# Kernel tuning notes

Hardware: AMD Instinct MI355X
Metric: run time of the kernel (lower is better)

The kernel has to match this reference:

```python
import jax, jax.numpy as jnp
import numpy as np

L = 0.24          # lambda step size
K = 0.03          # exp(log 0.03), conductance scale used by forward
NITER = 500       # ctor Niter
DEPS = 0.1


def _g(x, k):
    # Perona-Malik conductance: 1 / (1 + |x^2| / k^2); x real so |x*x| == x*x
    return 1.0 / (1.0 + (x * x) / (k * k))


def setup_inputs() -> dict:
    key = jax.random.key(0)
    k1, k2 = jax.random.split(key)
    guide = jax.random.normal(k1, (2, 3, 512, 512), dtype=jnp.float32)
    initial = jax.random.uniform(k2, (2, 1, 512, 512), dtype=jnp.float32)
    return {"guide": guide, "initial": initial}


def reference(guide, initial):
    # shift branch (jit-safe): forward adds deps if initial.min() <= deps, subtracts at end
    shift = jnp.where(jnp.min(initial) <= DEPS, DEPS, 0.0).astype(initial.dtype)
    depth0 = initial + shift

    # conductance coefficients from guide (mean abs channel gradient), shapes:
    # cv: [B,1,H-1,W], ch: [B,1,H,W-1]
    cv = _g(jnp.mean(jnp.abs(guide[:, :, 1:, :] - guide[:, :, :-1, :]), axis=1, keepdims=True), K)
    ch = _g(jnp.mean(jnp.abs(guide[:, :, :, 1:] - guide[:, :, :, :-1]), axis=1, keepdims=True), K)

    def step(I, _):
        # both diffs computed from the same I (matches torch: dv, dh read before writes;
        # the in-place +/- updates commute, so functional adds give identical math)
        dv = I[:, :, 1:, :] - I[:, :, :-1, :]
        dh = I[:, :, :, 1:] - I[:, :, :, :-1]
        tv = L * cv * dv
        th = L * ch * dh
        I = I.at[:, :, 1:, :].add(-tv)
        I = I.at[:, :, :-1, :].add(tv)
        I = I.at[:, :, :, 1:].add(-th)
        I = I.at[:, :, :, :-1].add(th)
        return I, None

    depth, _ = jax.lax.scan(step, depth0, None, length=NITER)
    y_pred = depth - shift
    return (y_pred, cv, ch)
```

## Files before the change

### kernel.cpp

```cpp
#include <hip/hip_runtime.h>


#define HH 512
#define WW 512
#define NB 2
static constexpr float LAM   = 0.24f;
static constexpr float KCOND = 0.03f;
static constexpr float DEPS_ = 0.1f;
static constexpr int IMG      = HH * WW;
static constexpr int N_DEPTH  = NB * IMG;
static constexpr int CV_PER_B = (HH - 1) * WW;
static constexpr int CH_PER_B = HH * (WW - 1);
static constexpr int N_CV     = NB * CV_PER_B;
static constexpr int N_CH     = NB * CH_PER_B;

static constexpr int T_FUSE = 10, NSS = 50;
static constexpr int TILE_W = 64, TILE_H = 32;
static constexpr int HALO_X = 12, HALO_Y = 10;
static constexpr int RW = TILE_W + 2 * HALO_X;
static constexpr int RH = TILE_H + 2 * HALO_Y;
static constexpr int NQ_ROW = RW / 4;
static constexpr int NQUAD  = NQ_ROW * RH;
static constexpr int SSZ    = (RH + 2) * RW;

static constexpr int NU_ROW = RW / 4;
static constexpr int NU_COL = RH / 2;
static constexpr int NUNIT  = NU_ROW * NU_COL;
static constexpr int NTF    = 576;

static constexpr int S_LDS    = 92;
static constexpr int ROWS_SZ  = (RH + 2) * S_LDS;
static constexpr int TRASH_OFF = ROWS_SZ;
static constexpr int EDGE_OFF = ROWS_SZ + S_LDS;
static constexpr int EDGE_ENT = 580;
static constexpr int BUF_SZ   = EDGE_OFF + EDGE_ENT * 4;

static constexpr int CVW = RW;
static constexpr int CV_SZ = (RH + 1) * CVW;
static constexpr int CHW = RW + 8;
static constexpr int CH_SZ = RH * CHW;
static constexpr int BLOB_BLK = CV_SZ + CH_SZ;

static constexpr int QPT_F = 5;

__device__ __forceinline__ unsigned fkey(float f) {
    unsigned u = __float_as_uint(f);
    return (u & 0x80000000u) ? ~u : (u | 0x80000000u);
}
__device__ __forceinline__ float kinv(unsigned k) {
    return __uint_as_float((k & 0x80000000u) ? (k & 0x7fffffffu) : ~k);
}

__global__ void init_key_kernel(unsigned* key) { *key = 0xFFFFFFFFu; }

__global__ void min_kernel(const float* __restrict__ x, unsigned* key) {
    float m = 3.4e38f;
    for (int idx = blockIdx.x * blockDim.x + threadIdx.x; idx < N_DEPTH;
         idx += gridDim.x * blockDim.x)
        m = fminf(m, x[idx]);
    for (int off = 32; off > 0; off >>= 1) m = fminf(m, __shfl_down(m, off, 64));
    __shared__ float sm[4];
    int lane = threadIdx.x & 63, wv = threadIdx.x >> 6;
    if (lane == 0) sm[wv] = m;
    __syncthreads();
    if (threadIdx.x == 0) {
        float mm = fminf(fminf(sm[0], sm[1]), fminf(sm[2], sm[3]));
        atomicMin(key, fkey(mm));
    }
}

__global__ void coeff_kernel(const float* __restrict__ g, float* __restrict__ cv,
                             float* __restrict__ chh) {
    int idx = blockIdx.x * blockDim.x + threadIdx.x;
    constexpr float kk = KCOND * KCOND;
    if (idx < N_CV) {
        int b = idx / CV_PER_B;
        int r = idx - b * CV_PER_B;
        int i = r >> 9, j = r & (WW - 1);
        const float* gb = g + b * 3 * IMG + i * WW + j;
        float s = 0.f;
#pragma unroll
        for (int c = 0; c < 3; ++c) s += fabsf(gb[c * IMG + WW] - gb[c * IMG]);
        float m = s / 3.0f;
        cv[idx] = 1.0f / (1.0f + (m * m) / kk);
    } else if (idx < N_CV + N_CH) {
        int t = idx - N_CV;
        int b = t / CH_PER_B;
        int r = t - b * CH_PER_B;
        int i = r / (WW - 1);
        int j = r - i * (WW - 1);
        const float* gb = g + b * 3 * IMG + i * WW + j;
        float s = 0.f;
#pragma unroll
        for (int c = 0; c < 3; ++c) s += fabsf(gb[c * IMG + 1] - gb[c * IMG]);
        float m = s / 3.0f;
        chh[t] = 1.0f / (1.0f + (m * m) / kk);
    }
}

__global__ __launch_bounds__(256) void prep_planes(const float* __restrict__ cv_g,
                                                   const float* __restrict__ ch_g,
                                                   float* __restrict__ blob) {
    const int blk = blockIdx.x;
    const int b   = blk >> 7, t = blk & 127;
    const int y0  = (t >> 3) * TILE_H;
    const int x0  = (t & 7) * TILE_W;
    const float* cvb = cv_g + b * CV_PER_B;
    const float* chb = ch_g + b * CH_PER_B;
    float* pv = blob + blk * BLOB_BLK;
    float* ph = pv + CV_SZ;
    for (int i = threadIdx.x; i < CV_SZ; i += 256) {
        int rr = i / CVW, x = i - rr * CVW;
        int gy = y0 - HALO_Y + rr, gx = x0 - HALO_X + x;
        bool ok = (rr >= 1) && (rr <= RH - 1) && (gy >= 1) && (gy <= HH - 1) &&
                  (gx >= 0) && (gx < WW);
        pv[i] = ok ? LAM * cvb[(gy - 1) * WW + gx] : 0.f;
    }
    for (int i = threadIdx.x; i < CH_SZ; i += 256) {
        int rr = i / CHW, xe = i - rr * CHW;
        int gy = y0 - HALO_Y + rr, gxe = x0 - HALO_X + xe;
        bool ok = (xe >= 1) && (xe <= RW - 1) && (gy >= 0) && (gy < HH) &&
                  (gxe >= 1) && (gxe < WW);
        ph[i] = ok ? LAM * chb[gy * (WW - 1) + (gxe - 1)] : 0.f;
    }
}

template <bool ADD_SHIFT, bool SUB_SHIFT>
__global__ __launch_bounds__(NTF, 1) void step_fast(
    const float* __restrict__ src, float* __restrict__ dst,
    const float* __restrict__ blob, const unsigned* __restrict__ key) {
    __shared__ float sb[2][BUF_SZ];
    const int blk = blockIdx.x;
    const int b   = blk >> 7, t = blk & 127;
    const int y0  = (t >> 3) * TILE_H;
    const int x0  = (t & 7) * TILE_W;
    const float* srcb = src + b * IMG;
    const float* pv   = blob + blk * BLOB_BLK;
    const float* ph   = pv + CV_SZ;

    float shift = 0.f;
    if (ADD_SHIFT || SUB_SHIFT) shift = (kinv(*key) <= DEPS_) ? DEPS_ : 0.f;
    const int tid = threadIdx.x;

    const bool act = tid < NUNIT;
    const int  uc  = act ? tid : 0;
    const int  pr  = uc / NU_ROW;
    const int  px  = uc - pr * NU_ROW;
    const int  x   = px * 4;
    const int  r0  = 2 * pr, r1 = r0 + 1;
    int roff0 = (r0 + 1) * S_LDS + x;
    int roff1 = roff0 + S_LDS;
    if (!act) {
        roff0 = TRASH_OFF + (tid & 3) * 8;
        roff1 = roff0 + 4;
    }
    const int e_w  = EDGE_OFF + (tid + 1) * 4;
    const int e_lf = EDGE_OFF + tid * 4 + 2;
    const int e_rt = EDGE_OFF + (tid + 2) * 4;

    const int gy0 = y0 - HALO_Y + r0, gy1 = gy0 + 1;
    const int gx  = x0 - HALO_X + x;
    const bool gx_in = (gx >= 0) && (gx <= WW - 4);
    const bool in0 = act && gx_in && (gy0 >= 0) && (gy0 < HH);
    const bool in1 = act && gx_in && (gy1 >= 0) && (gy1 < HH);
    const int goff0 = in0 ? (gy0 * WW + gx) : 0;
    const int goff1 = in1 ? (gy1 * WW + gx) : 0;
    const bool is_int = act && (r0 >= HALO_Y) && (r1 < HALO_Y + TILE_H) &&
                        (x >= HALO_X) && (x < HALO_X + TILE_W);

    const float am = act ? 1.f : 0.f;
    float ca[4], cm[4], cb[4], h0[5], h1[5];
    {
        float4 a = *reinterpret_cast<const float4*>(&pv[r0 * CVW + x]);
        float4 m = *reinterpret_cast<const float4*>(&pv[r1 * CVW + x]);
        float4 d = *reinterpret_cast<const float4*>(&pv[(r1 + 1) * CVW + x]);
        ca[0] = a.x * am; ca[1] = a.y * am; ca[2] = a.z * am; ca[3] = a.w * am;
        cm[0] = m.x * am; cm[1] = m.y * am; cm[2] = m.z * am; cm[3] = m.w * am;
        cb[0] = d.x * am; cb[1] = d.y * am; cb[2] = d.z * am; cb[3] = d.w * am;
        float4 u = *reinterpret_cast<const float4*>(&ph[r0 * CHW + x]);
        float  u4 = ph[r0 * CHW + x + 4];
        float4 w = *reinterpret_cast<const float4*>(&ph[r1 * CHW + x]);
        float  w4 = ph[r1 * CHW + x + 4];
        h0[0] = u.x * am; h0[1] = u.y * am; h0[2] = u.z * am; h0[3] = u.w * am; h0[4] = u4 * am;
        h1[0] = w.x * am; h1[1] = w.y * am; h1[2] = w.z * am; h1[3] = w.w * am; h1[4] = w4 * am;
    }

    float v0[4] = {0.f, 0.f, 0.f, 0.f}, v1[4] = {0.f, 0.f, 0.f, 0.f};
    if (in0) {
        float4 tv = *reinterpret_cast<const float4*>(srcb + goff0);
        if (ADD_SHIFT) { tv.x += shift; tv.y += shift; tv.z += shift; tv.w += shift; }
        v0[0] = tv.x; v0[1] = tv.y; v0[2] = tv.z; v0[3] = tv.w;
    }
    if (in1) {
        float4 tv = *reinterpret_cast<const float4*>(srcb + goff1);
        if (ADD_SHIFT) { tv.x += shift; tv.y += shift; tv.z += shift; tv.w += shift; }
        v1[0] = tv.x; v1[1] = tv.y; v1[2] = tv.z; v1[3] = tv.w;
    }

    for (int i = tid; i < S_LDS; i += NTF) {
        sb[0][i] = 0.f; sb[0][(RH + 1) * S_LDS + i] = 0.f;
        sb[1][i] = 0.f; sb[1][(RH + 1) * S_LDS + i] = 0.f;
    }
    if (tid == 0) {
        float4 z{0.f, 0.f, 0.f, 0.f};
        *reinterpret_cast<float4*>(&sb[0][EDGE_OFF]) = z;
        *reinterpret_cast<float4*>(&sb[1][EDGE_OFF]) = z;
        *reinterpret_cast<float4*>(&sb[0][EDGE_OFF + 577 * 4]) = z;
        *reinterpret_cast<float4*>(&sb[1][EDGE_OFF + 577 * 4]) = z;
    }
    *reinterpret_cast<float4*>(&sb[0][roff0]) = float4{v0[0], v0[1], v0[2], v0[3]};
    *reinterpret_cast<float4*>(&sb[0][roff1]) = float4{v1[0], v1[1], v1[2], v1[3]};
    *reinterpret_cast<float4*>(&sb[0][e_w])   = float4{v0[0], v1[0], v0[3], v1[3]};
    __syncthreads();

    int cur = 0;
    for (int it = 0; it < T_FUSE; ++it) {
        const float* s = sb[cur];
        float2 lfp = *reinterpret_cast<const float2*>(&s[e_lf]);
        float2 rtp = *reinterpret_cast<const float2*>(&s[e_rt]);
        float4 up = *reinterpret_cast<const float4*>(&s[roff0 - S_LDS]);
        float4 dn = *reinterpret_cast<const float4*>(&s[roff1 + S_LDS]);

        float n0[4], n1[4];
        n0[0] = v0[0] - ca[0] * (v0[0] - up.x) + cm[0] * (v1[0] - v0[0])
                      - h0[0] * (v0[0] - lfp.x) + h0[1] * (v0[1] - v0[0]);
        n0[1] = v0[1] - ca[1] * (v0[1] - up.y) + cm[1] * (v1[1] - v0[1])
                      - h0[1] * (v0[1] - v0[0]) + h0[2] * (v0[2] - v0[1]);
        n0[2] = v0[2] - ca[2] * (v0[2] - up.z) + cm[2] * (v1[2] - v0[2])
                      - h0[2] * (v0[2] - v0[1]) + h0[3] * (v0[3] - v0[2]);
        n0[3] = v0[3] - ca[3] * (v0[3] - up.w) + cm[3] * (v1[3] - v0[3])
                      - h0[3] * (v0[3] - v0[2]) + h0[4] * (rtp.x - v0[3]);
        n1[0] = v1[0] - cm[0] * (v1[0] - v0[0]) + cb[0] * (dn.x - v1[0])
                      - h1[0] * (v1[0] - lfp.y) + h1[1] * (v1[1] - v1[0]);
        n1[1] = v1[1] - cm[1] * (v1[1] - v0[1]) + cb[1] * (dn.y - v1[1])
                      - h1[1] * (v1[1] - v1[0]) + h1[2] * (v1[2] - v1[1]);
        n1[2] = v1[2] - cm[2] * (v1[2] - v0[2]) + cb[2] * (dn.z - v1[2])
                      - h1[2] * (v1[2] - v1[1]) + h1[3] * (v1[3] - v1[2]);
        n1[3] = v1[3] - cm[3] * (v1[3] - v0[3]) + cb[3] * (dn.w - v1[3])
                      - h1[3] * (v1[3] - v1[2]) + h1[4] * (rtp.y - v1[3]);

        int nxt = cur ^ 1;
        float* d = sb[nxt];
        *reinterpret_cast<float4*>(&d[roff0]) = float4{n0[0], n0[1], n0[2], n0[3]};
        *reinterpret_cast<float4*>(&d[roff1]) = float4{n1[0], n1[1], n1[2], n1[3]};
        *reinterpret_cast<float4*>(&d[e_w])   = float4{n0[0], n1[0], n0[3], n1[3]};
        v0[0] = n0[0]; v0[1] = n0[1]; v0[2] = n0[2]; v0[3] = n0[3];
        v1[0] = n1[0]; v1[1] = n1[1]; v1[2] = n1[2]; v1[3] = n1[3];
        cur = nxt;
        __syncthreads();
    }

    float* dstb = dst + b * IMG;
    if (is_int) {
        float4 o0{v0[0], v0[1], v0[2], v0[3]};
        float4 o1{v1[0], v1[1], v1[2], v1[3]};
        if (SUB_SHIFT) {
            o0.x -= shift; o0.y -= shift; o0.z -= shift; o0.w -= shift;
            o1.x -= shift; o1.y -= shift; o1.z -= shift; o1.w -= shift;
        }
        *reinterpret_cast<float4*>(dstb + goff0) = o0;
        *reinterpret_cast<float4*>(dstb + goff1) = o1;
    }
}

template <bool ADD_SHIFT, bool SUB_SHIFT>
__global__ __launch_bounds__(256, 1) void step_fused(
    const float* __restrict__ src, float* __restrict__ dst,
    const float* __restrict__ cv_g, const float* __restrict__ ch_g,
    const unsigned* __restrict__ key) {
    __shared__ float sb[2][SSZ];
    const int blk = blockIdx.x;
    const int b = blk >> 7, t = blk & 127;
    const int y0 = (t >> 3) * TILE_H, x0 = (t & 7) * TILE_W;
    const float* cvb = cv_g + b * CV_PER_B;
    const float* chb = ch_g + b * CH_PER_B;
    const float* srcb = src + b * IMG;
    float* dstb = dst + b * IMG;
    float shift = 0.f;
    if (ADD_SHIFT || SUB_SHIFT) shift = (kinv(*key) <= DEPS_) ? DEPS_ : 0.f;
    const int tid = threadIdx.x;
    float v[QPT_F][4], cu[QPT_F][4], cd[QPT_F][4], chq[QPT_F][5];
    int roff[QPT_F], rr[QPT_F], xx[QPT_F];
    bool act[QPT_F];
#pragma unroll
    for (int q = 0; q < QPT_F; ++q) {
        int qi = tid + q * 256;
        act[q] = qi < NQUAD;
        int qc = act[q] ? qi : 0;
        int r = qc / NQ_ROW;
        int x = (qc - r * NQ_ROW) * 4;
        rr[q] = r; xx[q] = x;
        roff[q] = (r + 1) * RW + x;
        int gy = y0 - HALO_Y + r, gx = x0 - HALO_X + x;
        bool gy_in = (gy >= 0) && (gy < HH);
#pragma unroll
        for (int j = 0; j < 4; ++j) {
            int gxx = gx + j;
            bool gx_in = (gxx >= 0) && (gxx < WW);
            bool vin = act[q] && gy_in && gx_in;
            float val = vin ? srcb[gy * WW + gxx] : 0.f;
            if (ADD_SHIFT) val += shift;
            v[q][j] = vin ? val : 0.f;
            bool up_ok = act[q] && (r >= 1) && (gy >= 1) && (gy < HH) && gx_in;
            cu[q][j] = up_ok ? LAM * cvb[(gy - 1) * WW + gxx] : 0.f;
            bool dn_ok = act[q] && (r <= RH - 2) && (gy >= 0) && (gy < HH - 1) && gx_in;
            cd[q][j] = dn_ok ? LAM * cvb[gy * WW + gxx] : 0.f;
        }
#pragma unroll
        for (int jj = 0; jj < 5; ++jj) {
            int xe = x + jj, gxe = gx + jj;
            bool ok = act[q] && (xe >= 1) && (xe <= RW - 1) && gy_in &&
                      (gxe >= 1) && (gxe < WW);
            chq[q][jj] = ok ? LAM * chb[gy * (WW - 1) + (gxe - 1)] : 0.f;
        }
    }
    for (int i = tid; i < RW; i += 256) {
        sb[0][i] = 0.f; sb[0][(RH + 1) * RW + i] = 0.f;
        sb[1][i] = 0.f; sb[1][(RH + 1) * RW + i] = 0.f;
    }
#pragma unroll
    for (int q = 0; q < QPT_F; ++q)
        if (act[q])
            *reinterpret_cast<float4*>(&sb[0][roff[q]]) =
                float4{v[q][0], v[q][1], v[q][2], v[q][3]};
    __syncthreads();
    int cur = 0;
    for (int it = 0; it < T_FUSE; ++it) {
        float nv[QPT_F][4];
#pragma unroll
        for (int q = 0; q < QPT_F; ++q) {
            const float* s = sb[cur];
            float4 up = *reinterpret_cast<const float4*>(&s[roff[q] - RW]);
            float4 dn = *reinterpret_cast<const float4*>(&s[roff[q] + RW]);
            float lf = s[roff[q] - 1];
            float rt = s[roff[q] + 4];
            float c0 = v[q][0], c1 = v[q][1], c2 = v[q][2], c3 = v[q][3];
            nv[q][0] = c0 - cu[q][0] * (c0 - up.x) + cd[q][0] * (dn.x - c0)
                          - chq[q][0] * (c0 - lf) + chq[q][1] * (c1 - c0);
            nv[q][1] = c1 - cu[q][1] * (c1 - up.y) + cd[q][1] * (dn.y - c1)
                          - chq[q][1] * (c1 - c0) + chq[q][2] * (c2 - c1);
            nv[q][2] = c2 - cu[q][2] * (c2 - up.z) + cd[q][2] * (dn.z - c2)
                          - chq[q][2] * (c2 - c1) + chq[q][3] * (c3 - c2);
            nv[q][3] = c3 - cu[q][3] * (c3 - up.w) + cd[q][3] * (dn.w - c3)
                          - chq[q][3] * (c3 - c2) + chq[q][4] * (rt - c3);
        }
        int nxt = cur ^ 1;
#pragma unroll
        for (int q = 0; q < QPT_F; ++q) {
            if (act[q])
                *reinterpret_cast<float4*>(&sb[nxt][roff[q]]) =
                    float4{nv[q][0], nv[q][1], nv[q][2], nv[q][3]};
            v[q][0] = nv[q][0]; v[q][1] = nv[q][1];
            v[q][2] = nv[q][2]; v[q][3] = nv[q][3];
        }
        cur = nxt;
        __syncthreads();
    }
#pragma unroll
    for (int q = 0; q < QPT_F; ++q) {
        if (!act[q]) continue;
        int r = rr[q], x = xx[q];
        if (r >= HALO_Y && r < HALO_Y + TILE_H && x >= HALO_X && x < HALO_X + TILE_W) {
            int gy = y0 - HALO_Y + r, gx = x0 - HALO_X + x;
            float4 o{v[q][0], v[q][1], v[q][2], v[q][3]};
            if (SUB_SHIFT) { o.x -= shift; o.y -= shift; o.z -= shift; o.w -= shift; }
            *reinterpret_cast<float4*>(dstb + gy * WW + gx) = o;
        }
    }
}

extern "C" void kernel_launch(void* const* d_in, const int* in_sizes, int n_in,
                              void* d_out, int out_size, void* d_ws, size_t ws_size,
                              hipStream_t stream) {
    const float* guide   = (const float*)d_in[0];
    const float* initial = (const float*)d_in[1];
    float* out    = (float*)d_out;
    float* out_y  = out;
    float* out_cv = out + N_DEPTH;
    float* out_ch = out + N_DEPTH + N_CV;

    unsigned* key = (unsigned*)d_ws;
    float* wsf    = (float*)d_ws;
    float* bufA   = wsf + 64;
    float* bufB   = bufA + N_DEPTH;
    float* blob   = bufB + N_DEPTH;

    const size_t need = (size_t)(64 + 2 * N_DEPTH + 256 * BLOB_BLK) * 4;
    const bool fast = ws_size >= need;

    hipLaunchKernelGGL(init_key_kernel, dim3(1), dim3(1), 0, stream, key);
    hipLaunchKernelGGL(min_kernel, dim3(256), dim3(256), 0, stream, initial, key);

    int nco = N_CV + N_CH;
    hipLaunchKernelGGL(coeff_kernel, dim3((nco + 255) / 256), dim3(256), 0, stream,
                       guide, out_cv, out_ch);
    if (fast)
        hipLaunchKernelGGL(prep_planes, dim3(256), dim3(256), 0, stream,
                           out_cv, out_ch, blob);

    float* bufs[2] = {bufA, bufB};
    for (int k = 0; k < NSS; ++k) {
        const float* src = (k == 0) ? initial : bufs[(k + 1) & 1];
        float*       dst = (k == NSS - 1) ? out_y : bufs[k & 1];
        if (fast) {
            if (k == 0)
                hipLaunchKernelGGL((step_fast<true, false>), dim3(256), dim3(NTF), 0,
                                   stream, src, dst, blob, key);
            else if (k == NSS - 1)
                hipLaunchKernelGGL((step_fast<false, true>), dim3(256), dim3(NTF), 0,
                                   stream, src, dst, blob, key);
            else
                hipLaunchKernelGGL((step_fast<false, false>), dim3(256), dim3(NTF), 0,
                                   stream, src, dst, blob, key);
        } else {
            if (k == 0)
                hipLaunchKernelGGL((step_fused<true, false>), dim3(256), dim3(256), 0,
                                   stream, src, dst, out_cv, out_ch, key);
            else if (k == NSS - 1)
                hipLaunchKernelGGL((step_fused<false, true>), dim3(256), dim3(256), 0,
                                   stream, src, dst, out_cv, out_ch, key);
            else
                hipLaunchKernelGGL((step_fused<false, false>), dim3(256), dim3(256), 0,
                                   stream, src, dst, out_cv, out_ch, key);
        }
    }
}
```

Baseline: 494.8 us.

## Replace per-superstep launches with persistent cooperative kernel using neighbor flags

Fuses the 50 superstep launches into one persistent cooperative kernel. Each tile block keeps its interior state and coefficients in registers, writes its interior to global memory with agent-scope stores, and waits on flag counters from its eight neighbour tiles before reloading only its halo. The min reduction and coefficient kernels are merged into one launch, and the precomputed coefficient blob is dropped in favour of direct gathers from the cv/ch outputs. The intent is to remove kernel launch gaps and redundant reloads of interior data. In exchange it adds spin-wait synchronisation, depends on all 256 blocks being co-resident, and falls back to the old per-step path if the cooperative launch fails.

```diff
diff --git a/kernel.cpp b/kernel.cpp
--- a/kernel.cpp
+++ b/kernel.cpp
@@ -35,12 +35,6 @@
 static constexpr int EDGE_ENT = 580;
 static constexpr int BUF_SZ   = EDGE_OFF + EDGE_ENT * 4;
 
-static constexpr int CVW = RW;
-static constexpr int CV_SZ = (RH + 1) * CVW;
-static constexpr int CHW = RW + 8;
-static constexpr int CH_SZ = RH * CHW;
-static constexpr int BLOB_BLK = CV_SZ + CH_SZ;
-
 static constexpr int QPT_F = 5;
 
 __device__ __forceinline__ unsigned fkey(float f) {
@@ -51,28 +45,48 @@
     return __uint_as_float((k & 0x80000000u) ? (k & 0x7fffffffu) : ~k);
 }
 
-__global__ void init_key_kernel(unsigned* key) { *key = 0xFFFFFFFFu; }
-
-__global__ void min_kernel(const float* __restrict__ x, unsigned* key) {
-    float m = 3.4e38f;
-    for (int idx = blockIdx.x * blockDim.x + threadIdx.x; idx < N_DEPTH;
-         idx += gridDim.x * blockDim.x)
-        m = fminf(m, x[idx]);
-    for (int off = 32; off > 0; off >>= 1) m = fminf(m, __shfl_down(m, off, 64));
-    __shared__ float sm[4];
-    int lane = threadIdx.x & 63, wv = threadIdx.x >> 6;
-    if (lane == 0) sm[wv] = m;
-    __syncthreads();
-    if (threadIdx.x == 0) {
-        float mm = fminf(fminf(sm[0], sm[1]), fminf(sm[2], sm[3]));
-        atomicMin(key, fkey(mm));
-    }
-}
-
-__global__ void coeff_kernel(const float* __restrict__ g, float* __restrict__ cv,
-                             float* __restrict__ chh) {
-    int idx = blockIdx.x * blockDim.x + threadIdx.x;
+__device__ __forceinline__ float2 cohload8(const float* p) {
+    unsigned long long u = __hip_atomic_load(
+        reinterpret_cast<const unsigned long long*>(p),
+        __ATOMIC_RELAXED, __HIP_MEMORY_SCOPE_AGENT);
+    union { unsigned long long u; float2 f; } c; c.u = u;
+    return c.f;
+}
+__device__ __forceinline__ void cohstore8(float* p, float a, float b) {
+    union { unsigned long long u; float f[2]; } c;
+    c.f[0] = a; c.f[1] = b;
+    __hip_atomic_store(reinterpret_cast<unsigned long long*>(p), c.u,
+                       __ATOMIC_RELAXED, __HIP_MEMORY_SCOPE_AGENT);
+}
+
+__global__ void init_key_kernel(unsigned* key, unsigned* flags) {
+    if (threadIdx.x == 0) *key = 0xFFFFFFFFu;
+    flags[threadIdx.x] = 0u;
+}
+
+static constexpr int NCO_BLK = (N_CV + N_CH + 255) / 256;
+__global__ void coeff_min_kernel(const float* __restrict__ g,
+                                 const float* __restrict__ ini,
+                                 float* __restrict__ cv, float* __restrict__ chh,
+                                 unsigned* __restrict__ key) {
     constexpr float kk = KCOND * KCOND;
+    if ((int)blockIdx.x >= NCO_BLK) {
+        int bid = blockIdx.x - NCO_BLK;
+        float m = 3.4e38f;
+        for (int idx = bid * 256 + threadIdx.x; idx < N_DEPTH; idx += 256 * 256)
+            m = fminf(m, ini[idx]);
+        for (int off = 32; off > 0; off >>= 1) m = fminf(m, __shfl_down(m, off, 64));
+        __shared__ float sm[4];
+        int lane = threadIdx.x & 63, wv = threadIdx.x >> 6;
+        if (lane == 0) sm[wv] = m;
+        __syncthreads();
+        if (threadIdx.x == 0) {
+            float mm = fminf(fminf(sm[0], sm[1]), fminf(sm[2], sm[3]));
+            atomicMin(key, fkey(mm));
+        }
+        return;
+    }
+    int idx = blockIdx.x * 256 + threadIdx.x;
     if (idx < N_CV) {
         int b = idx / CV_PER_B;
         int r = idx - b * CV_PER_B;
@@ -98,48 +112,18 @@
     }
 }
 
-__global__ __launch_bounds__(256) void prep_planes(const float* __restrict__ cv_g,
-                                                   const float* __restrict__ ch_g,
-                                                   float* __restrict__ blob) {
-    const int blk = blockIdx.x;
-    const int b   = blk >> 7, t = blk & 127;
-    const int y0  = (t >> 3) * TILE_H;
-    const int x0  = (t & 7) * TILE_W;
-    const float* cvb = cv_g + b * CV_PER_B;
-    const float* chb = ch_g + b * CH_PER_B;
-    float* pv = blob + blk * BLOB_BLK;
-    float* ph = pv + CV_SZ;
-    for (int i = threadIdx.x; i < CV_SZ; i += 256) {
-        int rr = i / CVW, x = i - rr * CVW;
-        int gy = y0 - HALO_Y + rr, gx = x0 - HALO_X + x;
-        bool ok = (rr >= 1) && (rr <= RH - 1) && (gy >= 1) && (gy <= HH - 1) &&
-                  (gx >= 0) && (gx < WW);
-        pv[i] = ok ? LAM * cvb[(gy - 1) * WW + gx] : 0.f;
-    }
-    for (int i = threadIdx.x; i < CH_SZ; i += 256) {
-        int rr = i / CHW, xe = i - rr * CHW;
-        int gy = y0 - HALO_Y + rr, gxe = x0 - HALO_X + xe;
-        bool ok = (xe >= 1) && (xe <= RW - 1) && (gy >= 0) && (gy < HH) &&
-                  (gxe >= 1) && (gxe < WW);
-        ph[i] = ok ? LAM * chb[gy * (WW - 1) + (gxe - 1)] : 0.f;
-    }
-}
-
-template <bool ADD_SHIFT, bool SUB_SHIFT>
-__global__ __launch_bounds__(NTF, 1) void step_fast(
-    const float* __restrict__ src, float* __restrict__ dst,
-    const float* __restrict__ blob, const unsigned* __restrict__ key) {
+__global__ __launch_bounds__(NTF, 1) void diffuse_persist(
+    const float* __restrict__ initial, float* __restrict__ out_y,
+    float* __restrict__ bufA, float* __restrict__ bufB,
+    const float* __restrict__ cv_g, const float* __restrict__ ch_g,
+    const unsigned* __restrict__ key, unsigned* __restrict__ flags) {
     __shared__ float sb[2][BUF_SZ];
     const int blk = blockIdx.x;
     const int b   = blk >> 7, t = blk & 127;
-    const int y0  = (t >> 3) * TILE_H;
-    const int x0  = (t & 7) * TILE_W;
-    const float* srcb = src + b * IMG;
-    const float* pv   = blob + blk * BLOB_BLK;
-    const float* ph   = pv + CV_SZ;
-
-    float shift = 0.f;
-    if (ADD_SHIFT || SUB_SHIFT) shift = (kinv(*key) <= DEPS_) ? DEPS_ : 0.f;
+    const int ty  = t >> 3, tx = t & 7;
+    const int y0  = ty * TILE_H;
+    const int x0  = tx * TILE_W;
+    const float shift = (kinv(*key) <= DEPS_) ? DEPS_ : 0.f;
     const int tid = threadIdx.x;
 
     const bool act = tid < NUNIT;
@@ -150,10 +134,7 @@
     const int  r0  = 2 * pr, r1 = r0 + 1;
     int roff0 = (r0 + 1) * S_LDS + x;
     int roff1 = roff0 + S_LDS;
-    if (!act) {
-        roff0 = TRASH_OFF + (tid & 3) * 8;
-        roff1 = roff0 + 4;
-    }
+    if (!act) { roff0 = TRASH_OFF + (tid & 3) * 8; roff1 = roff0 + 4; }
     const int e_w  = EDGE_OFF + (tid + 1) * 4;
     const int e_lf = EDGE_OFF + tid * 4 + 2;
     const int e_rt = EDGE_OFF + (tid + 2) * 4;
@@ -168,33 +149,48 @@
     const bool is_int = act && (r0 >= HALO_Y) && (r1 < HALO_Y + TILE_H) &&
                         (x >= HALO_X) && (x < HALO_X + TILE_W);
 
-    const float am = act ? 1.f : 0.f;
+    const float* cvb = cv_g + b * CV_PER_B;
+    const float* chb = ch_g + b * CH_PER_B;
     float ca[4], cm[4], cb[4], h0[5], h1[5];
-    {
-        float4 a = *reinterpret_cast<const float4*>(&pv[r0 * CVW + x]);
-        float4 m = *reinterpret_cast<const float4*>(&pv[r1 * CVW + x]);
-        float4 d = *reinterpret_cast<const float4*>(&pv[(r1 + 1) * CVW + x]);
-        ca[0] = a.x * am; ca[1] = a.y * am; ca[2] = a.z * am; ca[3] = a.w * am;
-        cm[0] = m.x * am; cm[1] = m.y * am; cm[2] = m.z * am; cm[3] = m.w * am;
-        cb[0] = d.x * am; cb[1] = d.y * am; cb[2] = d.z * am; cb[3] = d.w * am;
-        float4 u = *reinterpret_cast<const float4*>(&ph[r0 * CHW + x]);
-        float  u4 = ph[r0 * CHW + x + 4];
-        float4 w = *reinterpret_cast<const float4*>(&ph[r1 * CHW + x]);
-        float  w4 = ph[r1 * CHW + x + 4];
-        h0[0] = u.x * am; h0[1] = u.y * am; h0[2] = u.z * am; h0[3] = u.w * am; h0[4] = u4 * am;
-        h1[0] = w.x * am; h1[1] = w.y * am; h1[2] = w.z * am; h1[3] = w.w * am; h1[4] = w4 * am;
+#pragma unroll
+    for (int j = 0; j < 4; ++j) {
+        int gxx = gx + j;
+        bool gxo = (gxx >= 0) && (gxx < WW);
+        bool a_ok = act && (r0 >= 1) && (gy0 >= 1) && (gy0 <= HH - 1) && gxo;
+        ca[j] = a_ok ? LAM * cvb[(gy0 - 1) * WW + gxx] : 0.f;
+        bool m_ok = act && (gy1 >= 1) && (gy1 <= HH - 1) && gxo;
+        cm[j] = m_ok ? LAM * cvb[(gy1 - 1) * WW + gxx] : 0.f;
+        bool b_ok = act && (r1 <= RH - 2) && (gy1 + 1 >= 1) && (gy1 + 1 <= HH - 1) && gxo;
+        cb[j] = b_ok ? LAM * cvb[gy1 * WW + gxx] : 0.f;
+    }
+#pragma unroll
+    for (int jj = 0; jj < 5; ++jj) {
+        int xe = x + jj, gxe = gx + jj;
+        bool e_ok = (xe >= 1) && (xe <= RW - 1) && (gxe >= 1) && (gxe < WW);
+        bool ok0 = act && e_ok && (gy0 >= 0) && (gy0 < HH);
+        h0[jj] = ok0 ? LAM * chb[gy0 * (WW - 1) + (gxe - 1)] : 0.f;
+        bool ok1 = act && e_ok && (gy1 >= 0) && (gy1 < HH);
+        h1[jj] = ok1 ? LAM * chb[gy1 * (WW - 1) + (gxe - 1)] : 0.f;
+    }
+
+    int nbr = -1;
+    if (tid < 8) {
+        int d  = tid + (tid >= 4 ? 1 : 0);
+        int dy = d / 3 - 1, dx = d % 3 - 1;
+        int ny = ty + dy, nx = tx + dx;
+        if (ny >= 0 && ny < 16 && nx >= 0 && nx < 8)
+            nbr = (b << 7) + (ny << 3) + nx;
     }
 
     float v0[4] = {0.f, 0.f, 0.f, 0.f}, v1[4] = {0.f, 0.f, 0.f, 0.f};
+    const float* ib = initial + b * IMG;
     if (in0) {
-        float4 tv = *reinterpret_cast<const float4*>(srcb + goff0);
-        if (ADD_SHIFT) { tv.x += shift; tv.y += shift; tv.z += shift; tv.w += shift; }
-        v0[0] = tv.x; v0[1] = tv.y; v0[2] = tv.z; v0[3] = tv.w;
+        float4 tv = *reinterpret_cast<const float4*>(ib + goff0);
+        v0[0] = tv.x + shift; v0[1] = tv.y + shift; v0[2] = tv.z + shift; v0[3] = tv.w + shift;
     }
     if (in1) {
-        float4 tv = *reinterpret_cast<const float4*>(srcb + goff1);
-        if (ADD_SHIFT) { tv.x += shift; tv.y += shift; tv.z += shift; tv.w += shift; }
-        v1[0] = tv.x; v1[1] = tv.y; v1[2] = tv.z; v1[3] = tv.w;
+        float4 tv = *reinterpret_cast<const float4*>(ib + goff1);
+        v1[0] = tv.x + shift; v1[1] = tv.y + shift; v1[2] = tv.z + shift; v1[3] = tv.w + shift;
     }
 
     for (int i = tid; i < S_LDS; i += NTF) {
@@ -213,53 +209,90 @@
     *reinterpret_cast<float4*>(&sb[0][e_w])   = float4{v0[0], v1[0], v0[3], v1[3]};
     __syncthreads();
 
-    int cur = 0;
-    for (int it = 0; it < T_FUSE; ++it) {
-        const float* s = sb[cur];
-        float2 lfp = *reinterpret_cast<const float2*>(&s[e_lf]);
-        float2 rtp = *reinterpret_cast<const float2*>(&s[e_rt]);
-        float4 up = *reinterpret_cast<const float4*>(&s[roff0 - S_LDS]);
-        float4 dn = *reinterpret_cast<const float4*>(&s[roff1 + S_LDS]);
-
-        float n0[4], n1[4];
-        n0[0] = v0[0] - ca[0] * (v0[0] - up.x) + cm[0] * (v1[0] - v0[0])
-                      - h0[0] * (v0[0] - lfp.x) + h0[1] * (v0[1] - v0[0]);
-        n0[1] = v0[1] - ca[1] * (v0[1] - up.y) + cm[1] * (v1[1] - v0[1])
-                      - h0[1] * (v0[1] - v0[0]) + h0[2] * (v0[2] - v0[1]);
-        n0[2] = v0[2] - ca[2] * (v0[2] - up.z) + cm[2] * (v1[2] - v0[2])
-                      - h0[2] * (v0[2] - v0[1]) + h0[3] * (v0[3] - v0[2]);
-        n0[3] = v0[3] - ca[3] * (v0[3] - up.w) + cm[3] * (v1[3] - v0[3])
-                      - h0[3] * (v0[3] - v0[2]) + h0[4] * (rtp.x - v0[3]);
-        n1[0] = v1[0] - cm[0] * (v1[0] - v0[0]) + cb[0] * (dn.x - v1[0])
-                      - h1[0] * (v1[0] - lfp.y) + h1[1] * (v1[1] - v1[0]);
-        n1[1] = v1[1] - cm[1] * (v1[1] - v0[1]) + cb[1] * (dn.y - v1[1])
-                      - h1[1] * (v1[1] - v1[0]) + h1[2] * (v1[2] - v1[1]);
-        n1[2] = v1[2] - cm[2] * (v1[2] - v0[2]) + cb[2] * (dn.z - v1[2])
-                      - h1[2] * (v1[2] - v1[1]) + h1[3] * (v1[3] - v1[2]);
-        n1[3] = v1[3] - cm[3] * (v1[3] - v0[3]) + cb[3] * (dn.w - v1[3])
-                      - h1[3] * (v1[3] - v1[2]) + h1[4] * (rtp.y - v1[3]);
-
-        int nxt = cur ^ 1;
-        float* d = sb[nxt];
-        *reinterpret_cast<float4*>(&d[roff0]) = float4{n0[0], n0[1], n0[2], n0[3]};
-        *reinterpret_cast<float4*>(&d[roff1]) = float4{n1[0], n1[1], n1[2], n1[3]};
-        *reinterpret_cast<float4*>(&d[e_w])   = float4{n0[0], n1[0], n0[3], n1[3]};
-        v0[0] = n0[0]; v0[1] = n0[1]; v0[2] = n0[2]; v0[3] = n0[3];
-        v1[0] = n1[0]; v1[1] = n1[1]; v1[2] = n1[2]; v1[3] = n1[3];
-        cur = nxt;
-        __syncthreads();
-    }
-
-    float* dstb = dst + b * IMG;
-    if (is_int) {
-        float4 o0{v0[0], v0[1], v0[2], v0[3]};
-        float4 o1{v1[0], v1[1], v1[2], v1[3]};
-        if (SUB_SHIFT) {
-            o0.x -= shift; o0.y -= shift; o0.z -= shift; o0.w -= shift;
-            o1.x -= shift; o1.y -= shift; o1.z -= shift; o1.w -= shift;
-        }
-        *reinterpret_cast<float4*>(dstb + goff0) = o0;
-        *reinterpret_cast<float4*>(dstb + goff1) = o1;
+    for (int k = 0; k < NSS; ++k) {
+        if (k > 0) {
+            if (nbr >= 0) {
+                while (__hip_atomic_load(&flags[nbr], __ATOMIC_RELAXED,
+                                         __HIP_MEMORY_SCOPE_AGENT) < (unsigned)k) {}
+            }
+            __syncthreads();
+            asm volatile("" ::: "memory");
+            const float* srcb = ((k & 1) ? bufA : bufB) + b * IMG;
+            if (act && !is_int) {
+                float2 a0{0.f, 0.f}, b0{0.f, 0.f}, a1{0.f, 0.f}, b1{0.f, 0.f};
+                if (in0) { a0 = cohload8(srcb + goff0); b0 = cohload8(srcb + goff0 + 2); }
+                if (in1) { a1 = cohload8(srcb + goff1); b1 = cohload8(srcb + goff1 + 2); }
+                v0[0] = a0.x; v0[1] = a0.y; v0[2] = b0.x; v0[3] = b0.y;
+                v1[0] = a1.x; v1[1] = a1.y; v1[2] = b1.x; v1[3] = b1.y;
+                *reinterpret_cast<float4*>(&sb[0][roff0]) =
+                    float4{v0[0], v0[1], v0[2], v0[3]};
+                *reinterpret_cast<float4*>(&sb[0][roff1]) =
+                    float4{v1[0], v1[1], v1[2], v1[3]};
+                *reinterpret_cast<float4*>(&sb[0][e_w]) =
+                    float4{v0[0], v1[0], v0[3], v1[3]};
+            }
+            __syncthreads();
+        }
+
+        int cur = 0;
+        for (int it = 0; it < T_FUSE; ++it) {
+            const float* s = sb[cur];
+            float2 lfp = *reinterpret_cast<const float2*>(&s[e_lf]);
+            float2 rtp = *reinterpret_cast<const float2*>(&s[e_rt]);
+            float4 up = *reinterpret_cast<const float4*>(&s[roff0 - S_LDS]);
+            float4 dn = *reinterpret_cast<const float4*>(&s[roff1 + S_LDS]);
+
+            float n0[4], n1[4];
+            n0[0] = v0[0] - ca[0] * (v0[0] - up.x) + cm[0] * (v1[0] - v0[0])
+                          - h0[0] * (v0[0] - lfp.x) + h0[1] * (v0[1] - v0[0]);
+            n0[1] = v0[1] - ca[1] * (v0[1] - up.y) + cm[1] * (v1[1] - v0[1])
+                          - h0[1] * (v0[1] - v0[0]) + h0[2] * (v0[2] - v0[1]);
+            n0[2] = v0[2] - ca[2] * (v0[2] - up.z) + cm[2] * (v1[2] - v0[2])
+                          - h0[2] * (v0[2] - v0[1]) + h0[3] * (v0[3] - v0[2]);
+            n0[3] = v0[3] - ca[3] * (v0[3] - up.w) + cm[3] * (v1[3] - v0[3])
+                          - h0[3] * (v0[3] - v0[2]) + h0[4] * (rtp.x - v0[3]);
+            n1[0] = v1[0] - cm[0] * (v1[0] - v0[0]) + cb[0] * (dn.x - v1[0])
+                          - h1[0] * (v1[0] - lfp.y) + h1[1] * (v1[1] - v1[0]);
+            n1[1] = v1[1] - cm[1] * (v1[1] - v0[1]) + cb[1] * (dn.y - v1[1])
+                          - h1[1] * (v1[1] - v1[0]) + h1[2] * (v1[2] - v1[1]);
+            n1[2] = v1[2] - cm[2] * (v1[2] - v0[2]) + cb[2] * (dn.z - v1[2])
+                          - h1[2] * (v1[2] - v1[1]) + h1[3] * (v1[3] - v1[2]);
+            n1[3] = v1[3] - cm[3] * (v1[3] - v0[3]) + cb[3] * (dn.w - v1[3])
+                          - h1[3] * (v1[3] - v1[2]) + h1[4] * (rtp.y - v1[3]);
+
+            int nxt = cur ^ 1;
+            float* d = sb[nxt];
+            *reinterpret_cast<float4*>(&d[roff0]) = float4{n0[0], n0[1], n0[2], n0[3]};
+            *reinterpret_cast<float4*>(&d[roff1]) = float4{n1[0], n1[1], n1[2], n1[3]};
+            *reinterpret_cast<float4*>(&d[e_w])   = float4{n0[0], n1[0], n0[3], n1[3]};
+            v0[0] = n0[0]; v0[1] = n0[1]; v0[2] = n0[2]; v0[3] = n0[3];
+            v1[0] = n1[0]; v1[1] = n1[1]; v1[2] = n1[2]; v1[3] = n1[3];
+            cur = nxt;
+            __syncthreads();
+        }
+
+        if (k == NSS - 1) {
+            float* dstb = out_y + b * IMG;
+            if (is_int) {
+                float4 o0{v0[0] - shift, v0[1] - shift, v0[2] - shift, v0[3] - shift};
+                float4 o1{v1[0] - shift, v1[1] - shift, v1[2] - shift, v1[3] - shift};
+                *reinterpret_cast<float4*>(dstb + goff0) = o0;
+                *reinterpret_cast<float4*>(dstb + goff1) = o1;
+            }
+        } else {
+            float* dstb = ((k & 1) ? bufB : bufA) + b * IMG;
+            if (is_int) {
+                cohstore8(dstb + goff0,     v0[0], v0[1]);
+                cohstore8(dstb + goff0 + 2, v0[2], v0[3]);
+                cohstore8(dstb + goff1,     v1[0], v1[1]);
+                cohstore8(dstb + goff1 + 2, v1[2], v1[3]);
+            }
+            asm volatile("s_waitcnt vmcnt(0)" ::: "memory");
+            __syncthreads();
+            if (tid == 0)
+                __hip_atomic_store(&flags[blk], (unsigned)(k + 1),
+                                   __ATOMIC_RELAXED, __HIP_MEMORY_SCOPE_AGENT);
+        }
     }
 }
 
@@ -383,45 +416,43 @@
     float* wsf    = (float*)d_ws;
     float* bufA   = wsf + 64;
     float* bufB   = bufA + N_DEPTH;
-    float* blob   = bufB + N_DEPTH;
-
-    const size_t need = (size_t)(64 + 2 * N_DEPTH + 256 * BLOB_BLK) * 4;
+    unsigned* flags = (unsigned*)(bufB + N_DEPTH);
+
+    const size_t need = (size_t)(64 + 2 * N_DEPTH + 256) * 4;
     const bool fast = ws_size >= need;
 
-    hipLaunchKernelGGL(init_key_kernel, dim3(1), dim3(1), 0, stream, key);
-    hipLaunchKernelGGL(min_kernel, dim3(256), dim3(256), 0, stream, initial, key);
-
-    int nco = N_CV + N_CH;
-    hipLaunchKernelGGL(coeff_kernel, dim3((nco + 255) / 256), dim3(256), 0, stream,
-                       guide, out_cv, out_ch);
-    if (fast)
-        hipLaunchKernelGGL(prep_planes, dim3(256), dim3(256), 0, stream,
-                           out_cv, out_ch, blob);
+    hipLaunchKernelGGL(init_key_kernel, dim3(1), dim3(256), 0, stream, key,
+                       fast ? flags : (unsigned*)d_ws + 1);
+    hipLaunchKernelGGL(coeff_min_kernel, dim3(NCO_BLK + 256), dim3(256), 0, stream,
+                       guide, initial, out_cv, out_ch, key);
+
+    if (fast) {
+        const float* a0 = initial;
+        float* a1 = out_y;
+        float* a2 = bufA;
+        float* a3 = bufB;
+        const float* a4 = out_cv;
+        const float* a5 = out_ch;
+        const unsigned* a6 = key;
+        unsigned* a7 = flags;
+        void* kargs[] = {&a0, &a1, &a2, &a3, &a4, &a5, &a6, &a7};
+        hipError_t ce = hipLaunchCooperativeKernel(
+            (const void*)diffuse_persist, dim3(256), dim3(NTF), kargs, 0, stream);
+        if (ce == hipSuccess) return;
+    }
 
     float* bufs[2] = {bufA, bufB};
     for (int k = 0; k < NSS; ++k) {
         const float* src = (k == 0) ? initial : bufs[(k + 1) & 1];
         float*       dst = (k == NSS - 1) ? out_y : bufs[k & 1];
-        if (fast) {
-            if (k == 0)
-                hipLaunchKernelGGL((step_fast<true, false>), dim3(256), dim3(NTF), 0,
-                                   stream, src, dst, blob, key);
-            else if (k == NSS - 1)
-                hipLaunchKernelGGL((step_fast<false, true>), dim3(256), dim3(NTF), 0,
-                                   stream, src, dst, blob, key);
-            else
-                hipLaunchKernelGGL((step_fast<false, false>), dim3(256), dim3(NTF), 0,
-                                   stream, src, dst, blob, key);
-        } else {
-            if (k == 0)
-                hipLaunchKernelGGL((step_fused<true, false>), dim3(256), dim3(256), 0,
-                                   stream, src, dst, out_cv, out_ch, key);
-            else if (k == NSS - 1)
-                hipLaunchKernelGGL((step_fused<false, true>), dim3(256), dim3(256), 0,
-                                   stream, src, dst, out_cv, out_ch, key);
-            else
-                hipLaunchKernelGGL((step_fused<false, false>), dim3(256), dim3(256), 0,
-                                   stream, src, dst, out_cv, out_ch, key);
-        }
-    }
-}
+        if (k == 0)
+            hipLaunchKernelGGL((step_fused<true, false>), dim3(256), dim3(256), 0,
+                               stream, src, dst, out_cv, out_ch, key);
+        else if (k == NSS - 1)
+            hipLaunchKernelGGL((step_fused<false, true>), dim3(256), dim3(256), 0,
+                               stream, src, dst, out_cv, out_ch, key);
+        else
+            hipLaunchKernelGGL((step_fused<false, false>), dim3(256), dim3(256), 0,
+                               stream, src, dst, out_cv, out_ch, key);
+    }
+}
```

Result: faster. 470.3 us (-5.0%).
